# Kernel optimization log

Hardware: AMD Instinct MI355X
Metric: run time of the kernel (lower is better)

The kernel has to match this reference:

```python
import jax, jax.numpy as jnp
import numpy as np
from jax import lax

B, T, F = 4096, 100, 40
H_ENC, H_LAT, H_DEC = 64, 32, 64


def _lstm(x, Wih, Whh, b):
    """PyTorch-convention LSTM (gate order i,f,g,o), batch_first, zero init state.
    x: [B,T,Fin], Wih: [4H,Fin], Whh: [4H,H], b: [4H] (= b_ih + b_hh).
    Returns hidden sequence [B,T,H]."""
    H = Whh.shape[1]
    # precompute input contributions for all timesteps in one GEMM
    xg = jnp.einsum('btf,gf->btg', x, Wih) + b  # [B,T,4H]
    h0 = jnp.zeros((x.shape[0], H), dtype=x.dtype)
    c0 = jnp.zeros((x.shape[0], H), dtype=x.dtype)

    def step(carry, gx_t):
        h, c = carry
        gates = gx_t + h @ Whh.T  # [B,4H]
        i, f, g, o = jnp.split(gates, 4, axis=-1)
        c = jax.nn.sigmoid(f) * c + jax.nn.sigmoid(i) * jnp.tanh(g)
        h = jax.nn.sigmoid(o) * jnp.tanh(c)
        return (h, c), h

    _, hs = lax.scan(step, (h0, c0), jnp.swapaxes(xg, 0, 1))  # [T,B,H]
    return jnp.swapaxes(hs, 0, 1)


def setup_inputs() -> dict:
    key = jax.random.key(0)
    ks = jax.random.split(key, 8)
    s = 0.05
    return {
        'x': jax.random.normal(ks[0], (B, T, F), dtype=jnp.float32),
        'enc_Wih': jax.random.normal(ks[1], (4 * H_ENC, F), dtype=jnp.float32) * s,
        'enc_Whh': jax.random.normal(ks[2], (4 * H_ENC, H_ENC), dtype=jnp.float32) * s,
        'enc_b': jnp.zeros((4 * H_ENC,), dtype=jnp.float32),
        'lat_Wih': jax.random.normal(ks[3], (4 * H_LAT, H_ENC), dtype=jnp.float32) * s,
        'lat_Whh': jax.random.normal(ks[4], (4 * H_LAT, H_LAT), dtype=jnp.float32) * s,
        'lat_b': jnp.zeros((4 * H_LAT,), dtype=jnp.float32),
        'dec_Wih': jax.random.normal(ks[5], (4 * H_DEC, H_LAT), dtype=jnp.float32) * s,
        'dec_Whh': jax.random.normal(ks[6], (4 * H_DEC, H_DEC), dtype=jnp.float32) * s,
        'dec_b': jnp.zeros((4 * H_DEC,), dtype=jnp.float32),
        'out_W': jax.random.normal(ks[7], (F, H_DEC), dtype=jnp.float32) * s,
        'out_b': jnp.zeros((F,), dtype=jnp.float32),
    }


def reference(x, enc_Wih, enc_Whh, enc_b, lat_Wih, lat_Whh, lat_b,
              dec_Wih, dec_Whh, dec_b, out_W, out_b):
    h = _lstm(x, enc_Wih, enc_Whh, enc_b)                 # [B,T,64]
    last = h[:, -1:, :]                                   # [B,1,64]
    rep = jnp.broadcast_to(last, (h.shape[0], h.shape[1], last.shape[-1]))
    h = _lstm(rep, lat_Wih, lat_Whh, lat_b)               # [B,T,32]
    h = _lstm(h, dec_Wih, dec_Whh, dec_b)                 # [B,T,64]
    return jnp.einsum('bth,fh->btf', h, out_W) + out_b    # [B,T,40]
```

## Files before the change

### kernel.cpp

```cpp
#include <hip/hip_runtime.h>
#include <hip/hip_bf16.h>
#include <cstddef>

typedef __attribute__((ext_vector_type(8))) short bf16x8;
typedef __attribute__((ext_vector_type(4))) float f32x4;

#define MFMA(a, b, c) __builtin_amdgcn_mfma_f32_16x16x32_bf16((a), (b), (c), 0, 0, 0)

static __device__ __forceinline__ unsigned short f2bf(float f) {
  __hip_bfloat16 b = __float2bfloat16(f);
  return __builtin_bit_cast(unsigned short, b);
}
static __device__ __forceinline__ float bf2f(unsigned short h) {
  unsigned u = ((unsigned)h) << 16;
  return __builtin_bit_cast(float, u);
}
static __device__ __forceinline__ float fast_sig(float x) {
  return __builtin_amdgcn_rcpf(1.0f + __expf(-x));
}
static __device__ __forceinline__ float fast_tanh(float x) {
  return 2.0f * __builtin_amdgcn_rcpf(1.0f + __expf(-2.0f * x)) - 1.0f;
}

static __device__ __forceinline__ bf16x8 aread(const char* base, int lane, int kc) {
  int b = lane & 15, g = lane >> 4;
  int off = (kc * 64 + g * 16) ^ ((b & 7) << 4);
  return *(const bf16x8*)(base + b * 256 + off);
}
static __device__ __forceinline__ void awrite16(char* base, int b, int k, unsigned short v) {
  int off = (2 * k) ^ ((b & 7) << 4);
  *(unsigned short*)(base + b * 256 + off) = v;
}
static __device__ __forceinline__ void awrite32(char* base, int b, int k, unsigned v) {
  int off = (2 * k) ^ ((b & 7) << 4);
  *(unsigned*)(base + b * 256 + off) = v;
}

extern "C" __global__ __launch_bounds__(512, 2)
void lstm_ae_mfma3(const float* __restrict__ x,
                   const float* __restrict__ eWih, const float* __restrict__ eWhh, const float* __restrict__ eb,
                   const float* __restrict__ lWih, const float* __restrict__ lWhh, const float* __restrict__ lb,
                   const float* __restrict__ dWih, const float* __restrict__ dWhh, const float* __restrict__ db,
                   const float* __restrict__ oW,  const float* __restrict__ ob,
                   float* __restrict__ out)
{
  __shared__ __align__(16) char sAhi[2][4096];
  __shared__ __align__(16) char sAlo[2][4096];

  const int tid  = threadIdx.x;
  const int lane = tid & 63;
  const int w    = tid >> 6;
  const int c16  = lane & 15;
  const int p4   = lane >> 4;
  const int bbase = blockIdx.x * 16;

  {
    f32x4 z = {0.f, 0.f, 0.f, 0.f};
    *(f32x4*)(&sAhi[0][0] + tid * 16) = z;
    *(f32x4*)(&sAlo[0][0] + tid * 16) = z;
  }

  bf16x8 ewh[2][4], ewl[2][4];
  float ebias[2][4];
#pragma unroll
  for (int n = 0; n < 2; ++n) {
    int tr = c16;
    int u = w * 8 + (tr >> 2) * 2 + n;
    int ga = tr & 3;
#pragma unroll
    for (int r = 0; r < 4; ++r) ebias[n][r] = eb[r * 64 + (w * 8 + p4 * 2 + n)];
#pragma unroll
    for (int kc = 0; kc < 4; ++kc) {
      bf16x8 hi, lo;
#pragma unroll
      for (int e = 0; e < 8; ++e) {
        int k = kc * 32 + p4 * 8 + e;
        float v = 0.f;
        if (k < 40)       v = eWih[(ga * 64 + u) * 40 + k];
        else if (k >= 64) v = eWhh[(ga * 64 + u) * 64 + (k - 64)];
        unsigned short hh = f2bf(v);
        hi[e] = (short)hh;
        lo[e] = (short)f2bf(v - bf2f(hh));
      }
      ewh[n][kc] = hi; ewl[n][kc] = lo;
    }
  }

  __syncthreads();

  if (tid < 160) {
    int b = tid / 10, f4 = tid - b * 10;
    f32x4 ld = *(const f32x4*)(x + ((size_t)(bbase + b) * 100 + 0) * 40 + f4 * 4);
    unsigned long long ph = 0, pl = 0;
#pragma unroll
    for (int e = 0; e < 4; ++e) {
      unsigned short hh = f2bf(ld[e]);
      unsigned short ll = f2bf(ld[e] - bf2f(hh));
      ph |= (unsigned long long)hh << (16 * e);
      pl |= (unsigned long long)ll << (16 * e);
    }
    int off = (f4 * 8) ^ ((b & 7) << 4);
    *(unsigned long long*)(sAhi[0] + b * 256 + off) = ph;
    *(unsigned long long*)(sAlo[0] + b * 256 + off) = pl;
  }

  float cE[2] = {0.f, 0.f};
  int q = 0;
  __syncthreads();

#pragma unroll 1
  for (int t = 0; t < 100; ++t) {
    f32x4 xld;
    int sb = 0, sf4 = 0;
    const bool stager = (tid < 160);
    if (stager) {
      int tn = (t + 1 < 100) ? t + 1 : 99;
      sb = tid / 10; sf4 = tid - sb * 10;
      xld = *(const f32x4*)(x + ((size_t)(bbase + sb) * 100 + tn) * 40 + sf4 * 4);
    }

    f32x4 acc[2], acc2[2];
#pragma unroll
    for (int n = 0; n < 2; ++n) {
      acc[n]  = f32x4{ebias[n][0], ebias[n][1], ebias[n][2], ebias[n][3]};
      acc2[n] = f32x4{0.f, 0.f, 0.f, 0.f};
    }
    const char* Ah = sAhi[q];
    const char* Al = sAlo[q];
#pragma unroll
    for (int kc = 0; kc < 4; ++kc) {
      bf16x8 ah = aread(Ah, lane, kc);
      bf16x8 al = aread(Al, lane, kc);
#pragma unroll
      for (int n = 0; n < 2; ++n) {
        f32x4 t0 = (kc < 2) ? acc[n] : acc2[n];
        t0 = MFMA(ewh[n][kc], ah, t0);
        t0 = MFMA(ewl[n][kc], ah, t0);
        t0 = MFMA(ewh[n][kc], al, t0);
        if (kc < 2) acc[n] = t0; else acc2[n] = t0;
      }
    }

    char* AhN = sAhi[q ^ 1];
    char* AlN = sAlo[q ^ 1];
    unsigned short hh[2], hl[2];
#pragma unroll
    for (int n = 0; n < 2; ++n) {
      f32x4 gv = acc[n] + acc2[n];
      float ii = fast_sig(gv[0]), ff = fast_sig(gv[1]);
      float gg = fast_tanh(gv[2]), oo = fast_sig(gv[3]);
      cE[n] = ff * cE[n] + ii * gg;
      float hv = oo * fast_tanh(cE[n]);
      hh[n] = f2bf(hv);
      hl[n] = f2bf(hv - bf2f(hh[n]));
    }
    awrite32(AhN, c16, 64 + w * 8 + p4 * 2, (unsigned)hh[0] | ((unsigned)hh[1] << 16));
    awrite32(AlN, c16, 64 + w * 8 + p4 * 2, (unsigned)hl[0] | ((unsigned)hl[1] << 16));

    if (stager) {
      unsigned long long ph = 0, pl = 0;
#pragma unroll
      for (int e = 0; e < 4; ++e) {
        unsigned short hhx = f2bf(xld[e]);
        unsigned short llx = f2bf(xld[e] - bf2f(hhx));
        ph |= (unsigned long long)hhx << (16 * e);
        pl |= (unsigned long long)llx << (16 * e);
      }
      int off = (sf4 * 8) ^ ((sb & 7) << 4);
      *(unsigned long long*)(AhN + sb * 256 + off) = ph;
      *(unsigned long long*)(AlN + sb * 256 + off) = pl;
    }
    __syncthreads();
    q ^= 1;
  }

  f32x4 xga;
  {
    int tr = c16;
    int u = w * 4 + (tr >> 2), ga = tr & 3;
    int ul = w * 4 + p4;
    xga = f32x4{lb[ul], lb[32 + ul], lb[64 + ul], lb[96 + ul]};
#pragma unroll
    for (int kci = 0; kci < 2; ++kci) {
      bf16x8 hi, lo;
#pragma unroll
      for (int e = 0; e < 8; ++e) {
        float v = lWih[(ga * 32 + u) * 64 + kci * 32 + p4 * 8 + e];
        unsigned short hh = f2bf(v);
        hi[e] = (short)hh;
        lo[e] = (short)f2bf(v - bf2f(hh));
      }
      bf16x8 ah = aread(sAhi[q], lane, 2 + kci);
      bf16x8 al = aread(sAlo[q], lane, 2 + kci);
      xga = MFMA(hi, ah, xga);
      xga = MFMA(lo, ah, xga);
      xga = MFMA(hi, al, xga);
    }
  }
  __syncthreads();

  {
    f32x4 z = {0.f, 0.f, 0.f, 0.f};
    *(f32x4*)(&sAhi[0][0] + tid * 16) = z;
    *(f32x4*)(&sAlo[0][0] + tid * 16) = z;
  }

  bf16x8 lwh, lwl;
  {
    int tr = c16;
    int u = w * 4 + (tr >> 2), ga = tr & 3;
    bf16x8 hi, lo;
#pragma unroll
    for (int e = 0; e < 8; ++e) {
      float v = lWhh[(ga * 32 + u) * 32 + p4 * 8 + e];
      unsigned short hh = f2bf(v);
      hi[e] = (short)hh;
      lo[e] = (short)f2bf(v - bf2f(hh));
    }
    lwh = hi; lwl = lo;
  }
  bf16x8 dwh[2][3], dwl[2][3];
  float dbias[2][4];
#pragma unroll
  for (int n = 0; n < 2; ++n) {
    int tr = c16;
    int u = w * 8 + (tr >> 2) * 2 + n;
    int ga = tr & 3;
#pragma unroll
    for (int r = 0; r < 4; ++r) dbias[n][r] = db[r * 64 + (w * 8 + p4 * 2 + n)];
#pragma unroll
    for (int kc = 0; kc < 3; ++kc) {
      bf16x8 hi, lo;
#pragma unroll
      for (int e = 0; e < 8; ++e) {
        int k = kc * 32 + p4 * 8 + e;
        float v = (k < 32) ? dWih[(ga * 64 + u) * 32 + k]
                           : dWhh[(ga * 64 + u) * 64 + (k - 32)];
        unsigned short hh = f2bf(v);
        hi[e] = (short)hh;
        lo[e] = (short)f2bf(v - bf2f(hh));
      }
      dwh[n][kc] = hi; dwl[n][kc] = lo;
    }
  }
  bf16x8 pwh[2], pwl[2];
  float pbias[4];
#pragma unroll
  for (int r = 0; r < 4; ++r) {
    int f = w * 16 + p4 * 4 + r;
    pbias[r] = (w < 3 && f < 40) ? ob[f] : 0.0f;
  }
  if (w < 3) {
    int f = w * 16 + c16;
#pragma unroll
    for (int kci = 0; kci < 2; ++kci) {
      bf16x8 hi, lo;
#pragma unroll
      for (int e = 0; e < 8; ++e) {
        float v = (f < 40) ? oW[f * 64 + kci * 32 + p4 * 8 + e] : 0.0f;
        unsigned short hh = f2bf(v);
        hi[e] = (short)hh;
        lo[e] = (short)f2bf(v - bf2f(hh));
      }
      pwh[kci] = hi; pwl[kci] = lo;
    }
  }

  float cL = 0.f;
  float cD[2] = {0.f, 0.f};
  __syncthreads();

#pragma unroll 1
  for (int i = 0; i < 102; ++i) {
    const int pa = i & 1;
    bf16x8 c0h = aread(sAhi[pa ^ 1], lane, 0), c0l = aread(sAlo[pa ^ 1], lane, 0);
    bf16x8 d1h = aread(sAhi[pa], lane, 1),     d1l = aread(sAlo[pa], lane, 1);
    bf16x8 d2h = aread(sAhi[pa], lane, 2),     d2l = aread(sAlo[pa], lane, 2);

    if (i < 100) {
      f32x4 lac = xga;
      lac = MFMA(lwh, c0h, lac);
      lac = MFMA(lwl, c0h, lac);
      lac = MFMA(lwh, c0l, lac);
      float ii = fast_sig(lac[0]), ff = fast_sig(lac[1]);
      float gg = fast_tanh(lac[2]), oo = fast_sig(lac[3]);
      cL = ff * cL + ii * gg;
      float hv = oo * fast_tanh(cL);
      unsigned short hhh = f2bf(hv);
      awrite16(sAhi[pa], c16, w * 4 + p4, hhh);
      awrite16(sAlo[pa], c16, w * 4 + p4, f2bf(hv - bf2f(hhh)));
    }

    if (i >= 1 && i < 101) {
      unsigned short hh[2], hl[2];
#pragma unroll
      for (int n = 0; n < 2; ++n) {
        f32x4 dac = f32x4{dbias[n][0], dbias[n][1], dbias[n][2], dbias[n][3]};
        dac = MFMA(dwh[n][0], c0h, dac);
        dac = MFMA(dwl[n][0], c0h, dac);
        dac = MFMA(dwh[n][0], c0l, dac);
        dac = MFMA(dwh[n][1], d1h, dac);
        dac = MFMA(dwl[n][1], d1h, dac);
        dac = MFMA(dwh[n][1], d1l, dac);
        dac = MFMA(dwh[n][2], d2h, dac);
        dac = MFMA(dwl[n][2], d2h, dac);
        dac = MFMA(dwh[n][2], d2l, dac);
        float ii = fast_sig(dac[0]), ff = fast_sig(dac[1]);
        float gg = fast_tanh(dac[2]), oo = fast_sig(dac[3]);
        cD[n] = ff * cD[n] + ii * gg;
        float hv = oo * fast_tanh(cD[n]);
        hh[n] = f2bf(hv);
        hl[n] = f2bf(hv - bf2f(hh[n]));
      }
      awrite32(sAhi[pa ^ 1], c16, 32 + w * 8 + p4 * 2, (unsigned)hh[0] | ((unsigned)hh[1] << 16));
      awrite32(sAlo[pa ^ 1], c16, 32 + w * 8 + p4 * 2, (unsigned)hl[0] | ((unsigned)hl[1] << 16));
    }

    if (i >= 2 && w < 3) {
      f32x4 pac = f32x4{pbias[0], pbias[1], pbias[2], pbias[3]};
      pac = MFMA(pwh[0], d1h, pac);
      pac = MFMA(pwl[0], d1h, pac);
      pac = MFMA(pwh[0], d1l, pac);
      pac = MFMA(pwh[1], d2h, pac);
      pac = MFMA(pwl[1], d2h, pac);
      pac = MFMA(pwh[1], d2l, pac);
#pragma unroll
      for (int r = 0; r < 4; ++r) {
        int f = w * 16 + p4 * 4 + r;
        if (f < 40)
          out[((size_t)(bbase + c16) * 100 + (i - 2)) * 40 + f] = pac[r];
      }
    }
    __syncthreads();
  }
}

extern "C" void kernel_launch(void* const* d_in, const int* in_sizes, int n_in,
                              void* d_out, int out_size, void* d_ws, size_t ws_size,
                              hipStream_t stream) {
  const float* x    = (const float*)d_in[0];
  const float* eWih = (const float*)d_in[1];
  const float* eWhh = (const float*)d_in[2];
  const float* eb   = (const float*)d_in[3];
  const float* lWih = (const float*)d_in[4];
  const float* lWhh = (const float*)d_in[5];
  const float* lb   = (const float*)d_in[6];
  const float* dWih = (const float*)d_in[7];
  const float* dWhh = (const float*)d_in[8];
  const float* db   = (const float*)d_in[9];
  const float* oW   = (const float*)d_in[10];
  const float* ob   = (const float*)d_in[11];
  float* out = (float*)d_out;

  lstm_ae_mfma3<<<256, 512, 0, stream>>>(x, eWih, eWhh, eb, lWih, lWhh, lb,
                                         dWih, dWhh, db, oW, ob, out);
}
```

Measured before the change: 181.5 us.

## Precompute next-step encoder input gates off the recurrent critical path

The encoder loop now computes the x-projection for step t+1 alongside the recurrent h-projection for step t. The dependent chain per step shrinks from 12 chained MFMAs to two 3-MFMA chains. x is staged two steps ahead. Decoder and projection MFMA chains are split into independent partial accumulators that are summed at the end, which shortens dependency latency. A hand-written round-to-nearest-even bf16 conversion replaces the library call. The change adds register pressure from the extra accumulators and alters the buffer indexing after the loop.

```diff
diff --git a/kernel.cpp b/kernel.cpp
--- a/kernel.cpp
+++ b/kernel.cpp
@@ -1,5 +1,4 @@
 #include <hip/hip_runtime.h>
-#include <hip/hip_bf16.h>
 #include <cstddef>
 
 typedef __attribute__((ext_vector_type(8))) short bf16x8;
@@ -8,8 +7,9 @@
 #define MFMA(a, b, c) __builtin_amdgcn_mfma_f32_16x16x32_bf16((a), (b), (c), 0, 0, 0)
 
 static __device__ __forceinline__ unsigned short f2bf(float f) {
-  __hip_bfloat16 b = __float2bfloat16(f);
-  return __builtin_bit_cast(unsigned short, b);
+  unsigned u = __builtin_bit_cast(unsigned, f);
+  u = u + 0x7FFFu + ((u >> 16) & 1u);
+  return (unsigned short)(u >> 16);
 }
 static __device__ __forceinline__ float bf2f(unsigned short h) {
   unsigned u = ((unsigned)h) << 16;
@@ -37,7 +37,7 @@
 }
 
 extern "C" __global__ __launch_bounds__(512, 2)
-void lstm_ae_mfma3(const float* __restrict__ x,
+void lstm_ae_mfma4(const float* __restrict__ x,
                    const float* __restrict__ eWih, const float* __restrict__ eWhh, const float* __restrict__ eb,
                    const float* __restrict__ lWih, const float* __restrict__ lWhh, const float* __restrict__ lb,
                    const float* __restrict__ dWih, const float* __restrict__ dWhh, const float* __restrict__ db,
@@ -88,9 +88,11 @@
 
   __syncthreads();
 
-  if (tid < 160) {
-    int b = tid / 10, f4 = tid - b * 10;
-    f32x4 ld = *(const f32x4*)(x + ((size_t)(bbase + b) * 100 + 0) * 40 + f4 * 4);
+  if (tid < 320) {
+    int s = (tid < 160) ? tid : tid - 160;
+    int buf = (tid < 160) ? 0 : 1;
+    int b = s / 10, f4 = s - b * 10;
+    f32x4 ld = *(const f32x4*)(x + ((size_t)(bbase + b) * 100 + buf) * 40 + f4 * 4);
     unsigned long long ph = 0, pl = 0;
 #pragma unroll
     for (int e = 0; e < 4; ++e) {
@@ -100,62 +102,86 @@
       pl |= (unsigned long long)ll << (16 * e);
     }
     int off = (f4 * 8) ^ ((b & 7) << 4);
-    *(unsigned long long*)(sAhi[0] + b * 256 + off) = ph;
-    *(unsigned long long*)(sAlo[0] + b * 256 + off) = pl;
-  }
+    *(unsigned long long*)(sAhi[buf] + b * 256 + off) = ph;
+    *(unsigned long long*)(sAlo[buf] + b * 256 + off) = pl;
+  }
+  __syncthreads();
+
+  f32x4 xg[2];
+  {
+    bf16x8 x0h = aread(sAhi[0], lane, 0), x0l = aread(sAlo[0], lane, 0);
+    bf16x8 x1h = aread(sAhi[0], lane, 1), x1l = aread(sAlo[0], lane, 1);
+#pragma unroll
+    for (int n = 0; n < 2; ++n) {
+      f32x4 a = f32x4{ebias[n][0], ebias[n][1], ebias[n][2], ebias[n][3]};
+      a = MFMA(ewh[n][0], x0h, a);
+      a = MFMA(ewl[n][0], x0h, a);
+      a = MFMA(ewh[n][0], x0l, a);
+      f32x4 b = f32x4{0.f, 0.f, 0.f, 0.f};
+      b = MFMA(ewh[n][1], x1h, b);
+      b = MFMA(ewl[n][1], x1h, b);
+      b = MFMA(ewh[n][1], x1l, b);
+      xg[n] = a + b;
+    }
+  }
+  __syncthreads();
 
   float cE[2] = {0.f, 0.f};
-  int q = 0;
-  __syncthreads();
 
 #pragma unroll 1
   for (int t = 0; t < 100; ++t) {
+    const int cb = t & 1;
+    const char* Rh = sAhi[cb ^ 1];
+    const char* Rl = sAlo[cb ^ 1];
+    char* Wh = sAhi[cb];
+    char* Wl = sAlo[cb];
+
+    bf16x8 x0h = aread(Rh, lane, 0), x0l = aread(Rl, lane, 0);
+    bf16x8 x1h = aread(Rh, lane, 1), x1l = aread(Rl, lane, 1);
+    bf16x8 h2h = aread(Rh, lane, 2), h2l = aread(Rl, lane, 2);
+    bf16x8 h3h = aread(Rh, lane, 3), h3l = aread(Rl, lane, 3);
+
     f32x4 xld;
-    int sb = 0, sf4 = 0;
-    const bool stager = (tid < 160);
-    if (stager) {
-      int tn = (t + 1 < 100) ? t + 1 : 99;
-      sb = tid / 10; sf4 = tid - sb * 10;
-      xld = *(const f32x4*)(x + ((size_t)(bbase + sb) * 100 + tn) * 40 + sf4 * 4);
-    }
-
-    f32x4 acc[2], acc2[2];
+    const bool stager = (tid < 160) && (t + 2 < 100);
+    int sb = tid / 10, sf4 = tid - sb * 10;
+    if (stager)
+      xld = *(const f32x4*)(x + ((size_t)(bbase + sb) * 100 + (t + 2)) * 40 + sf4 * 4);
+
+    f32x4 xnA[2], xnB[2], haA[2], haB[2];
 #pragma unroll
     for (int n = 0; n < 2; ++n) {
-      acc[n]  = f32x4{ebias[n][0], ebias[n][1], ebias[n][2], ebias[n][3]};
-      acc2[n] = f32x4{0.f, 0.f, 0.f, 0.f};
-    }
-    const char* Ah = sAhi[q];
-    const char* Al = sAlo[q];
-#pragma unroll
-    for (int kc = 0; kc < 4; ++kc) {
-      bf16x8 ah = aread(Ah, lane, kc);
-      bf16x8 al = aread(Al, lane, kc);
-#pragma unroll
-      for (int n = 0; n < 2; ++n) {
-        f32x4 t0 = (kc < 2) ? acc[n] : acc2[n];
-        t0 = MFMA(ewh[n][kc], ah, t0);
-        t0 = MFMA(ewl[n][kc], ah, t0);
-        t0 = MFMA(ewh[n][kc], al, t0);
-        if (kc < 2) acc[n] = t0; else acc2[n] = t0;
-      }
-    }
-
-    char* AhN = sAhi[q ^ 1];
-    char* AlN = sAlo[q ^ 1];
+      haA[n] = xg[n];
+      haA[n] = MFMA(ewh[n][2], h2h, haA[n]);
+      haA[n] = MFMA(ewl[n][2], h2h, haA[n]);
+      haA[n] = MFMA(ewh[n][2], h2l, haA[n]);
+      haB[n] = f32x4{0.f, 0.f, 0.f, 0.f};
+      haB[n] = MFMA(ewh[n][3], h3h, haB[n]);
+      haB[n] = MFMA(ewl[n][3], h3h, haB[n]);
+      haB[n] = MFMA(ewh[n][3], h3l, haB[n]);
+      xnA[n] = f32x4{ebias[n][0], ebias[n][1], ebias[n][2], ebias[n][3]};
+      xnA[n] = MFMA(ewh[n][0], x0h, xnA[n]);
+      xnA[n] = MFMA(ewl[n][0], x0h, xnA[n]);
+      xnA[n] = MFMA(ewh[n][0], x0l, xnA[n]);
+      xnB[n] = f32x4{0.f, 0.f, 0.f, 0.f};
+      xnB[n] = MFMA(ewh[n][1], x1h, xnB[n]);
+      xnB[n] = MFMA(ewl[n][1], x1h, xnB[n]);
+      xnB[n] = MFMA(ewh[n][1], x1l, xnB[n]);
+    }
+
     unsigned short hh[2], hl[2];
 #pragma unroll
     for (int n = 0; n < 2; ++n) {
-      f32x4 gv = acc[n] + acc2[n];
+      f32x4 gv = haA[n] + haB[n];
       float ii = fast_sig(gv[0]), ff = fast_sig(gv[1]);
       float gg = fast_tanh(gv[2]), oo = fast_sig(gv[3]);
       cE[n] = ff * cE[n] + ii * gg;
       float hv = oo * fast_tanh(cE[n]);
       hh[n] = f2bf(hv);
       hl[n] = f2bf(hv - bf2f(hh[n]));
-    }
-    awrite32(AhN, c16, 64 + w * 8 + p4 * 2, (unsigned)hh[0] | ((unsigned)hh[1] << 16));
-    awrite32(AlN, c16, 64 + w * 8 + p4 * 2, (unsigned)hl[0] | ((unsigned)hl[1] << 16));
+      xg[n] = xnA[n] + xnB[n];
+    }
+    awrite32(Wh, c16, 64 + w * 8 + p4 * 2, (unsigned)hh[0] | ((unsigned)hh[1] << 16));
+    awrite32(Wl, c16, 64 + w * 8 + p4 * 2, (unsigned)hl[0] | ((unsigned)hl[1] << 16));
 
     if (stager) {
       unsigned long long ph = 0, pl = 0;
@@ -167,11 +193,10 @@
         pl |= (unsigned long long)llx << (16 * e);
       }
       int off = (sf4 * 8) ^ ((sb & 7) << 4);
-      *(unsigned long long*)(AhN + sb * 256 + off) = ph;
-      *(unsigned long long*)(AlN + sb * 256 + off) = pl;
+      *(unsigned long long*)(Wh + sb * 256 + off) = ph;
+      *(unsigned long long*)(Wl + sb * 256 + off) = pl;
     }
     __syncthreads();
-    q ^= 1;
   }
 
   f32x4 xga;
@@ -190,8 +215,8 @@
         hi[e] = (short)hh;
         lo[e] = (short)f2bf(v - bf2f(hh));
       }
-      bf16x8 ah = aread(sAhi[q], lane, 2 + kci);
-      bf16x8 al = aread(sAlo[q], lane, 2 + kci);
+      bf16x8 ah = aread(sAhi[1], lane, 2 + kci);
+      bf16x8 al = aread(sAlo[1], lane, 2 + kci);
       xga = MFMA(hi, ah, xga);
       xga = MFMA(lo, ah, xga);
       xga = MFMA(hi, al, xga);
@@ -295,18 +320,21 @@
       unsigned short hh[2], hl[2];
 #pragma unroll
       for (int n = 0; n < 2; ++n) {
-        f32x4 dac = f32x4{dbias[n][0], dbias[n][1], dbias[n][2], dbias[n][3]};
-        dac = MFMA(dwh[n][0], c0h, dac);
-        dac = MFMA(dwl[n][0], c0h, dac);
-        dac = MFMA(dwh[n][0], c0l, dac);
-        dac = MFMA(dwh[n][1], d1h, dac);
-        dac = MFMA(dwl[n][1], d1h, dac);
-        dac = MFMA(dwh[n][1], d1l, dac);
-        dac = MFMA(dwh[n][2], d2h, dac);
-        dac = MFMA(dwl[n][2], d2h, dac);
-        dac = MFMA(dwh[n][2], d2l, dac);
-        float ii = fast_sig(dac[0]), ff = fast_sig(dac[1]);
-        float gg = fast_tanh(dac[2]), oo = fast_sig(dac[3]);
+        f32x4 dA = f32x4{dbias[n][0], dbias[n][1], dbias[n][2], dbias[n][3]};
+        dA = MFMA(dwh[n][0], c0h, dA);
+        dA = MFMA(dwl[n][0], c0h, dA);
+        dA = MFMA(dwh[n][0], c0l, dA);
+        f32x4 dB = f32x4{0.f, 0.f, 0.f, 0.f};
+        dB = MFMA(dwh[n][1], d1h, dB);
+        dB = MFMA(dwl[n][1], d1h, dB);
+        dB = MFMA(dwh[n][1], d1l, dB);
+        f32x4 dC = f32x4{0.f, 0.f, 0.f, 0.f};
+        dC = MFMA(dwh[n][2], d2h, dC);
+        dC = MFMA(dwl[n][2], d2h, dC);
+        dC = MFMA(dwh[n][2], d2l, dC);
+        f32x4 gv = (dA + dB) + dC;
+        float ii = fast_sig(gv[0]), ff = fast_sig(gv[1]);
+        float gg = fast_tanh(gv[2]), oo = fast_sig(gv[3]);
         cD[n] = ff * cD[n] + ii * gg;
         float hv = oo * fast_tanh(cD[n]);
         hh[n] = f2bf(hv);
@@ -317,13 +345,15 @@
     }
 
     if (i >= 2 && w < 3) {
-      f32x4 pac = f32x4{pbias[0], pbias[1], pbias[2], pbias[3]};
-      pac = MFMA(pwh[0], d1h, pac);
-      pac = MFMA(pwl[0], d1h, pac);
-      pac = MFMA(pwh[0], d1l, pac);
-      pac = MFMA(pwh[1], d2h, pac);
-      pac = MFMA(pwl[1], d2h, pac);
-      pac = MFMA(pwh[1], d2l, pac);
+      f32x4 pA = f32x4{pbias[0], pbias[1], pbias[2], pbias[3]};
+      pA = MFMA(pwh[0], d1h, pA);
+      pA = MFMA(pwl[0], d1h, pA);
+      pA = MFMA(pwh[0], d1l, pA);
+      f32x4 pB = f32x4{0.f, 0.f, 0.f, 0.f};
+      pB = MFMA(pwh[1], d2h, pB);
+      pB = MFMA(pwl[1], d2h, pB);
+      pB = MFMA(pwh[1], d2l, pB);
+      f32x4 pac = pA + pB;
 #pragma unroll
       for (int r = 0; r < 4; ++r) {
         int f = w * 16 + p4 * 4 + r;
@@ -352,6 +382,6 @@
   const float* ob   = (const float*)d_in[11];
   float* out = (float*)d_out;
 
-  lstm_ae_mfma3<<<256, 512, 0, stream>>>(x, eWih, eWhh, eb, lWih, lWhh, lb,
+  lstm_ae_mfma4<<<256, 512, 0, stream>>>(x, eWih, eWhh, eb, lWih, lWhh, lb,
                                          dWih, dWhh, db, oW, ob, out);
 }
```

Result: slower. 199.0 us (+9.6%).

## Prefetch encoder inputs two steps ahead and use LDS-only barriers

Applied to the files above, without the earlier changes.

Replaces __syncthreads with an inline s_waitcnt lgkmcnt(0) + s_barrier so barriers no longer wait on outstanding global loads or stores. The encoder loop is unrolled by two with explicit ping-pong buffers, and the x prefetch is issued two timesteps ahead so global load latency can overlap a full step. The f32-to-bf16 conversion is replaced with a manual round-to-nearest-even bit trick. Skipping the vmcnt wait relies on the compiler inserting its own waits before loaded registers are used, and the manual rounding does not handle NaN.

```diff
diff --git a/kernel.cpp b/kernel.cpp
--- a/kernel.cpp
+++ b/kernel.cpp
@@ -1,5 +1,4 @@
 #include <hip/hip_runtime.h>
-#include <hip/hip_bf16.h>
 #include <cstddef>
 
 typedef __attribute__((ext_vector_type(8))) short bf16x8;
@@ -8,8 +7,9 @@
 #define MFMA(a, b, c) __builtin_amdgcn_mfma_f32_16x16x32_bf16((a), (b), (c), 0, 0, 0)
 
 static __device__ __forceinline__ unsigned short f2bf(float f) {
-  __hip_bfloat16 b = __float2bfloat16(f);
-  return __builtin_bit_cast(unsigned short, b);
+  unsigned u = __builtin_bit_cast(unsigned, f);
+  u = u + 0x7FFFu + ((u >> 16) & 1u);
+  return (unsigned short)(u >> 16);
 }
 static __device__ __forceinline__ float bf2f(unsigned short h) {
   unsigned u = ((unsigned)h) << 16;
@@ -20,6 +20,10 @@
 }
 static __device__ __forceinline__ float fast_tanh(float x) {
   return 2.0f * __builtin_amdgcn_rcpf(1.0f + __expf(-2.0f * x)) - 1.0f;
+}
+
+static __device__ __forceinline__ void lds_barrier() {
+  asm volatile("s_waitcnt lgkmcnt(0)\n\ts_barrier" ::: "memory");
 }
 
 static __device__ __forceinline__ bf16x8 aread(const char* base, int lane, int kc) {
@@ -37,7 +41,7 @@
 }
 
 extern "C" __global__ __launch_bounds__(512, 2)
-void lstm_ae_mfma3(const float* __restrict__ x,
+void lstm_ae_mfma5(const float* __restrict__ x,
                    const float* __restrict__ eWih, const float* __restrict__ eWhh, const float* __restrict__ eb,
                    const float* __restrict__ lWih, const float* __restrict__ lWhh, const float* __restrict__ lb,
                    const float* __restrict__ dWih, const float* __restrict__ dWhh, const float* __restrict__ db,
@@ -86,11 +90,12 @@
     }
   }
 
-  __syncthreads();
-
-  if (tid < 160) {
-    int b = tid / 10, f4 = tid - b * 10;
-    f32x4 ld = *(const f32x4*)(x + ((size_t)(bbase + b) * 100 + 0) * 40 + f4 * 4);
+  lds_barrier();
+
+  const bool stager = (tid < 160);
+  const int sb = tid / 10, sf4 = tid - (tid / 10) * 10;
+  if (stager) {
+    f32x4 ld = *(const f32x4*)(x + ((size_t)(bbase + sb) * 100 + 0) * 40 + sf4 * 4);
     unsigned long long ph = 0, pl = 0;
 #pragma unroll
     for (int e = 0; e < 4; ++e) {
@@ -99,24 +104,33 @@
       ph |= (unsigned long long)hh << (16 * e);
       pl |= (unsigned long long)ll << (16 * e);
     }
-    int off = (f4 * 8) ^ ((b & 7) << 4);
-    *(unsigned long long*)(sAhi[0] + b * 256 + off) = ph;
-    *(unsigned long long*)(sAlo[0] + b * 256 + off) = pl;
-  }
+    int off = (sf4 * 8) ^ ((sb & 7) << 4);
+    *(unsigned long long*)(sAhi[0] + sb * 256 + off) = ph;
+    *(unsigned long long*)(sAlo[0] + sb * 256 + off) = pl;
+  }
+  f32x4 xldA = {0.f, 0.f, 0.f, 0.f}, xldB = {0.f, 0.f, 0.f, 0.f};
+  if (stager)
+    xldA = *(const f32x4*)(x + ((size_t)(bbase + sb) * 100 + 1) * 40 + sf4 * 4);
 
   float cE[2] = {0.f, 0.f};
-  int q = 0;
-  __syncthreads();
-
-#pragma unroll 1
-  for (int t = 0; t < 100; ++t) {
-    f32x4 xld;
-    int sb = 0, sf4 = 0;
-    const bool stager = (tid < 160);
+  lds_barrier();
+
+  auto enc_step = [&](int t, const char* Rh, const char* Rl, char* Wh, char* Wl,
+                      f32x4& xin, f32x4& xout) {
     if (stager) {
-      int tn = (t + 1 < 100) ? t + 1 : 99;
-      sb = tid / 10; sf4 = tid - sb * 10;
-      xld = *(const f32x4*)(x + ((size_t)(bbase + sb) * 100 + tn) * 40 + sf4 * 4);
+      unsigned long long ph = 0, pl = 0;
+#pragma unroll
+      for (int e = 0; e < 4; ++e) {
+        unsigned short hh = f2bf(xin[e]);
+        unsigned short ll = f2bf(xin[e] - bf2f(hh));
+        ph |= (unsigned long long)hh << (16 * e);
+        pl |= (unsigned long long)ll << (16 * e);
+      }
+      int off = (sf4 * 8) ^ ((sb & 7) << 4);
+      *(unsigned long long*)(Wh + sb * 256 + off) = ph;
+      *(unsigned long long*)(Wl + sb * 256 + off) = pl;
+      int tn = (t + 2 <= 99) ? t + 2 : 99;
+      xout = *(const f32x4*)(x + ((size_t)(bbase + sb) * 100 + tn) * 40 + sf4 * 4);
     }
 
     f32x4 acc[2], acc2[2];
@@ -125,12 +139,10 @@
       acc[n]  = f32x4{ebias[n][0], ebias[n][1], ebias[n][2], ebias[n][3]};
       acc2[n] = f32x4{0.f, 0.f, 0.f, 0.f};
     }
-    const char* Ah = sAhi[q];
-    const char* Al = sAlo[q];
 #pragma unroll
     for (int kc = 0; kc < 4; ++kc) {
-      bf16x8 ah = aread(Ah, lane, kc);
-      bf16x8 al = aread(Al, lane, kc);
+      bf16x8 ah = aread(Rh, lane, kc);
+      bf16x8 al = aread(Rl, lane, kc);
 #pragma unroll
       for (int n = 0; n < 2; ++n) {
         f32x4 t0 = (kc < 2) ? acc[n] : acc2[n];
@@ -141,8 +153,6 @@
       }
     }
 
-    char* AhN = sAhi[q ^ 1];
-    char* AlN = sAlo[q ^ 1];
     unsigned short hh[2], hl[2];
 #pragma unroll
     for (int n = 0; n < 2; ++n) {
@@ -154,24 +164,16 @@
       hh[n] = f2bf(hv);
       hl[n] = f2bf(hv - bf2f(hh[n]));
     }
-    awrite32(AhN, c16, 64 + w * 8 + p4 * 2, (unsigned)hh[0] | ((unsigned)hh[1] << 16));
-    awrite32(AlN, c16, 64 + w * 8 + p4 * 2, (unsigned)hl[0] | ((unsigned)hl[1] << 16));
-
-    if (stager) {
-      unsigned long long ph = 0, pl = 0;
-#pragma unroll
-      for (int e = 0; e < 4; ++e) {
-        unsigned short hhx = f2bf(xld[e]);
-        unsigned short llx = f2bf(xld[e] - bf2f(hhx));
-        ph |= (unsigned long long)hhx << (16 * e);
-        pl |= (unsigned long long)llx << (16 * e);
-      }
-      int off = (sf4 * 8) ^ ((sb & 7) << 4);
-      *(unsigned long long*)(AhN + sb * 256 + off) = ph;
-      *(unsigned long long*)(AlN + sb * 256 + off) = pl;
-    }
-    __syncthreads();
-    q ^= 1;
+    awrite32(Wh, c16, 64 + w * 8 + p4 * 2, (unsigned)hh[0] | ((unsigned)hh[1] << 16));
+    awrite32(Wl, c16, 64 + w * 8 + p4 * 2, (unsigned)hl[0] | ((unsigned)hl[1] << 16));
+
+    lds_barrier();
+  };
+
+#pragma unroll 1
+  for (int tt = 0; tt < 100; tt += 2) {
+    enc_step(tt,     sAhi[0], sAlo[0], sAhi[1], sAlo[1], xldA, xldB);
+    enc_step(tt + 1, sAhi[1], sAlo[1], sAhi[0], sAlo[0], xldB, xldA);
   }
 
   f32x4 xga;
@@ -190,14 +192,14 @@
         hi[e] = (short)hh;
         lo[e] = (short)f2bf(v - bf2f(hh));
       }
-      bf16x8 ah = aread(sAhi[q], lane, 2 + kci);
-      bf16x8 al = aread(sAlo[q], lane, 2 + kci);
+      bf16x8 ah = aread(sAhi[0], lane, 2 + kci);
+      bf16x8 al = aread(sAlo[0], lane, 2 + kci);
       xga = MFMA(hi, ah, xga);
       xga = MFMA(lo, ah, xga);
       xga = MFMA(hi, al, xga);
     }
   }
-  __syncthreads();
+  lds_barrier();
 
   {
     f32x4 z = {0.f, 0.f, 0.f, 0.f};
@@ -268,7 +270,7 @@
 
   float cL = 0.f;
   float cD[2] = {0.f, 0.f};
-  __syncthreads();
+  lds_barrier();
 
 #pragma unroll 1
   for (int i = 0; i < 102; ++i) {
@@ -331,7 +333,7 @@
           out[((size_t)(bbase + c16) * 100 + (i - 2)) * 40 + f] = pac[r];
       }
     }
-    __syncthreads();
+    lds_barrier();
   }
 }
 
@@ -352,6 +354,6 @@
   const float* ob   = (const float*)d_in[11];
   float* out = (float*)d_out;
 
-  lstm_ae_mfma3<<<256, 512, 0, stream>>>(x, eWih, eWhh, eb, lWih, lWhh, lb,
+  lstm_ae_mfma5<<<256, 512, 0, stream>>>(x, eWih, eWhh, eb, lWih, lWhh, lb,
                                          dWih, dWhh, db, oW, ob, out);
 }
```

Result: no change. 184.1 us (+1.4%).
